# Optimization experiments

Measured on AMD Instinct MI355X. Metric: run time of the kernel, lower is better.

The kernel has to match this reference:

```python
import jax, jax.numpy as jnp
import numpy as np

B, S, T = 64, 512, 256  # batch, seq_len, num_tags


def setup_inputs() -> dict:
    key = jax.random.key(0)
    k1, k2, k3, k4 = jax.random.split(key, 4)
    emissions = jax.random.normal(k1, (B, S, T), dtype=jnp.float32)
    tags = jax.random.randint(k2, (B, S), 0, T, dtype=jnp.int32)
    mask = jnp.ones((B, S), dtype=bool)
    # nn.init.uniform_(-0.01, 0.01) as in reset_parameters()
    transitions = jax.random.uniform(k3, (T, T), minval=-0.01, maxval=0.01, dtype=jnp.float32)
    tse = jax.random.uniform(k4, (T + 2, T + 2), minval=-0.01, maxval=0.01, dtype=jnp.float32)
    tse = tse.at[T + 1, T].set(-10000.0)  # transitions[end_tag, start_tag] = -10000
    return {"emissions": emissions, "tags": tags, "mask": mask,
            "transitions": transitions, "transitions_with_start_end": tse}


def reference(emissions, tags, mask, transitions, transitions_with_start_end):
    Bv, Sv, Tv = emissions.shape
    start, end = Tv, Tv + 1

    # ---- forward algorithm (log partition), faithful to the torch recurrence:
    # new[b, j] = alpha[b, j] + logsumexp_k( trans[k, j] + emit_t[b, k] )
    # (the mask line fv*mask + fv*~mask in the original is a no-op)
    alpha0 = emissions[:, 0] + transitions_with_start_end[start, :Tv]

    def step(alpha, em_t):  # em_t: [B, T]
        lse = jax.nn.logsumexp(transitions[None, :, :] + em_t[:, :, None], axis=1)  # [B, T]
        return alpha + lse, None

    ems = jnp.swapaxes(emissions[:, 1:], 0, 1)  # [S-1, B, T]
    alpha, _ = jax.lax.scan(step, alpha0, ems)
    forward_score = jax.nn.logsumexp(alpha + transitions_with_start_end[:Tv, end], axis=1)  # [B]

    # ---- gold path score
    mf = mask.astype(emissions.dtype)
    emit = jnp.take_along_axis(emissions, tags[:, :, None].astype(jnp.int32), axis=2)[:, :, 0]  # [B, S]
    score = transitions_with_start_end[start, tags[:, 0]]
    score = score + jnp.sum(emit * mf, axis=1)
    score = score + jnp.sum(transitions[tags[:, 1:], tags[:, :-1]] * mf[:, 1:], axis=1)
    last_idx = jnp.sum(mask.astype(jnp.int32), axis=1) - 1  # [B]
    last_tags = jnp.take_along_axis(tags, last_idx[:, None], axis=1)[:, 0]
    score = score + transitions_with_start_end[last_tags, end]

    return forward_score - score  # negative log-likelihood per batch element, [B]
```

## Files before the change

### kernel.cpp

```cpp
#include <hip/hip_runtime.h>
#include <cstdint>

#define B_ 64
#define S_ 512
#define T_ 256
#define TP2 258

#define BM 64
#define BK 32
#define LDA 40
#define LDB 40

typedef __attribute__((ext_vector_type(8))) short short8;
typedef __attribute__((ext_vector_type(4))) float f32x4;

__device__ __forceinline__ ushort f2bf(float f) {
    union { float f; uint32_t u; } c; c.f = f;
    uint32_t u = c.u;
    u += 0x7FFFu + ((u >> 16) & 1u);
    return (ushort)(u >> 16);
}

__global__ void prep_w(const float* __restrict__ trans, ushort* __restrict__ wt,
                       float* __restrict__ accb) {
    int k = blockIdx.x;
    int n = threadIdx.x;
    wt[n * T_ + k] = f2bf(__expf(trans[k * T_ + n]));
    if (k < B_) accb[k * T_ + n] = 0.f;
}

__global__ __launch_bounds__(256, 3) void gemm_lse(
    const float* __restrict__ em, const ushort* __restrict__ wt,
    float* __restrict__ accb)
{
    __shared__ ushort Alds[BM * LDA];
    __shared__ ushort Blds[T_ * LDB];

    int blk  = blockIdx.x;
    long r0  = (long)blk * BM;
    int batch = blk >> 3;
    bool has_s0 = (blk & 7) == 0;

    int tid  = threadIdx.x;
    int wave = tid >> 6;
    int lane = tid & 63;
    int quad = lane >> 4;
    int l15  = lane & 15;

    f32x4 acc[4][4];
    #pragma unroll
    for (int i = 0; i < 4; ++i)
        #pragma unroll
        for (int j = 0; j < 4; ++j)
            acc[i][j] = (f32x4){0.f, 0.f, 0.f, 0.f};

    int srow = tid >> 2;
    int skc  = (tid & 3) * 8;

    for (int kt = 0; kt < T_ / BK; ++kt) {
        int k0 = kt * BK;
        {
            const float* src = em + (r0 + srow) * T_ + k0 + skc;
            float4 va = *(const float4*)(src);
            float4 vb = *(const float4*)(src + 4);
            union { ushort u[8]; uint4 v; } pk;
            pk.u[0] = f2bf(__expf(va.x)); pk.u[1] = f2bf(__expf(va.y));
            pk.u[2] = f2bf(__expf(va.z)); pk.u[3] = f2bf(__expf(va.w));
            pk.u[4] = f2bf(__expf(vb.x)); pk.u[5] = f2bf(__expf(vb.y));
            pk.u[6] = f2bf(__expf(vb.z)); pk.u[7] = f2bf(__expf(vb.w));
            *(uint4*)&Alds[srow * LDA + skc] = pk.v;
        }
        #pragma unroll
        for (int p = 0; p < 4; ++p) {
            int idx = tid + p * 256;
            uint4 v = *(const uint4*)&wt[(idx >> 2) * T_ + k0 + (idx & 3) * 8];
            *(uint4*)&Blds[(idx >> 2) * LDB + (idx & 3) * 8] = v;
        }
        __syncthreads();

        short8 af[4], bf[4];
        #pragma unroll
        for (int i = 0; i < 4; ++i)
            af[i] = *(const short8*)&Alds[(i * 16 + l15) * LDA + quad * 8];
        #pragma unroll
        for (int j = 0; j < 4; ++j)
            bf[j] = *(const short8*)&Blds[(wave * 64 + j * 16 + l15) * LDB + quad * 8];
        #pragma unroll
        for (int i = 0; i < 4; ++i)
            #pragma unroll
            for (int j = 0; j < 4; ++j)
                acc[i][j] = __builtin_amdgcn_mfma_f32_16x16x32_bf16(af[i], bf[j], acc[i][j], 0, 0, 0);
        __syncthreads();
    }

    #pragma unroll
    for (int j = 0; j < 4; ++j) {
        float s = 0.f;
        #pragma unroll
        for (int i = 0; i < 4; ++i) {
            f32x4 a = acc[i][j];
            #pragma unroll
            for (int v = 0; v < 4; ++v) {
                bool skip = has_s0 && (i == 0) && (quad == 0) && (v == 0);
                if (!skip) s += __logf(a[v]);
            }
        }
        s += __shfl_xor(s, 16);
        s += __shfl_xor(s, 32);
        if (lane < 16)
            atomicAdd(&accb[batch * T_ + wave * 64 + j * 16 + lane], s);
    }
}

__global__ __launch_bounds__(256) void finalize(
    const float* __restrict__ em, const int* __restrict__ tags,
    const float* __restrict__ trans, const float* __restrict__ tse,
    const float* __restrict__ accb, float* __restrict__ out)
{
    __shared__ float red[8];
    int b = blockIdx.x;
    int j = threadIdx.x;
    int w = j >> 6;

    float v = em[(long)b * S_ * T_ + j] + tse[T_ * TP2 + j]
            + accb[b * T_ + j] + tse[j * TP2 + (T_ + 1)];

    float m = v;
    #pragma unroll
    for (int o = 32; o; o >>= 1) m = fmaxf(m, __shfl_xor(m, o));
    if ((j & 63) == 0) red[w] = m;
    __syncthreads();
    m = fmaxf(fmaxf(red[0], red[1]), fmaxf(red[2], red[3]));

    float e = __expf(v - m);
    #pragma unroll
    for (int o = 32; o; o >>= 1) e += __shfl_xor(e, o);
    if ((j & 63) == 0) red[4 + w] = e;
    __syncthreads();
    float fwd = m + __logf(red[4] + red[5] + red[6] + red[7]);

    const int* tg = tags + b * S_;
    float sc = 0.f;
    for (int s = j; s < S_; s += 256) {
        int t = tg[s];
        sc += em[((long)b * S_ + s) * T_ + t];
        if (s >= 1) sc += trans[t * T_ + tg[s - 1]];
    }
    if (j == 0) {
        sc += tse[T_ * TP2 + tg[0]];
        sc += tse[tg[S_ - 1] * TP2 + (T_ + 1)];
    }
    #pragma unroll
    for (int o = 32; o; o >>= 1) sc += __shfl_xor(sc, o);
    __syncthreads();
    if ((j & 63) == 0) red[w] = sc;
    __syncthreads();
    if (j == 0) out[b] = fwd - (red[0] + red[1] + red[2] + red[3]);
}

extern "C" void kernel_launch(void* const* d_in, const int* in_sizes, int n_in,
                              void* d_out, int out_size, void* d_ws, size_t ws_size,
                              hipStream_t stream) {
    const float* em    = (const float*)d_in[0];
    const int*   tags  = (const int*)d_in[1];
    const float* trans = (const float*)d_in[3];
    const float* tse   = (const float*)d_in[4];
    float* out = (float*)d_out;

    ushort* wt   = (ushort*)d_ws;
    float*  accb = (float*)((char*)d_ws + 131072);

    prep_w<<<T_, T_, 0, stream>>>(trans, wt, accb);
    gemm_lse<<<(B_ * S_) / BM, 256, 0, stream>>>(em, wt, accb);
    finalize<<<B_, T_, 0, stream>>>(em, tags, trans, tse, accb, out);
}
```

Before: 93.21 us.

## Double-buffer A tile in LDS and load B fragments directly from global

The GEMM main loop now double-buffers the exponentiated emission tile in shared memory. The next tile's global load and exp conversion overlap with the MFMAs on the current tile, which leaves one barrier per iteration instead of two. The B (exp-transition) fragments are read straight from global/L2 into registers, so the B shared-memory staging is gone. The loop is fully unrolled and the occupancy hint drops from 3 to 2 blocks per CU. This trades LDS traffic and barriers for more register pressure and uncoalesced-per-lane global reads of the weight matrix.

```diff
diff --git a/kernel.cpp b/kernel.cpp
--- a/kernel.cpp
+++ b/kernel.cpp
@@ -9,7 +9,6 @@
 #define BM 64
 #define BK 32
 #define LDA 40
-#define LDB 40
 
 typedef __attribute__((ext_vector_type(8))) short short8;
 typedef __attribute__((ext_vector_type(4))) float f32x4;
@@ -29,12 +28,11 @@
     if (k < B_) accb[k * T_ + n] = 0.f;
 }
 
-__global__ __launch_bounds__(256, 3) void gemm_lse(
+__global__ __launch_bounds__(256, 2) void gemm_lse(
     const float* __restrict__ em, const ushort* __restrict__ wt,
     float* __restrict__ accb)
 {
-    __shared__ ushort Alds[BM * LDA];
-    __shared__ ushort Blds[T_ * LDB];
+    __shared__ ushort Alds[2][BM * LDA];
 
     int blk  = blockIdx.x;
     long r0  = (long)blk * BM;
@@ -57,39 +55,56 @@
     int srow = tid >> 2;
     int skc  = (tid & 3) * 8;
 
-    for (int kt = 0; kt < T_ / BK; ++kt) {
-        int k0 = kt * BK;
-        {
-            const float* src = em + (r0 + srow) * T_ + k0 + skc;
-            float4 va = *(const float4*)(src);
-            float4 vb = *(const float4*)(src + 4);
+    const float*  asrc = em + (r0 + srow) * T_ + skc;
+    const ushort* bsrc = wt + (wave * 64 + l15) * T_ + quad * 8;
+
+    {
+        float4 va = *(const float4*)(asrc);
+        float4 vb = *(const float4*)(asrc + 4);
+        union { ushort u[8]; uint4 v; } pk;
+        pk.u[0] = f2bf(__expf(va.x)); pk.u[1] = f2bf(__expf(va.y));
+        pk.u[2] = f2bf(__expf(va.z)); pk.u[3] = f2bf(__expf(va.w));
+        pk.u[4] = f2bf(__expf(vb.x)); pk.u[5] = f2bf(__expf(vb.y));
+        pk.u[6] = f2bf(__expf(vb.z)); pk.u[7] = f2bf(__expf(vb.w));
+        *(uint4*)&Alds[0][srow * LDA + skc] = pk.v;
+    }
+    __syncthreads();
+
+    #pragma unroll
+    for (int kt = 0; kt < 8; ++kt) {
+        const int k0  = kt * BK;
+        const int cur = kt & 1;
+
+        short8 bf[4];
+        #pragma unroll
+        for (int j = 0; j < 4; ++j)
+            bf[j] = *(const short8*)(bsrc + j * 16 * T_ + k0);
+
+        float4 va, vb;
+        if (kt < 7) {
+            va = *(const float4*)(asrc + k0 + BK);
+            vb = *(const float4*)(asrc + k0 + BK + 4);
+        }
+
+        short8 af[4];
+        #pragma unroll
+        for (int i = 0; i < 4; ++i)
+            af[i] = *(const short8*)&Alds[cur][(i * 16 + l15) * LDA + quad * 8];
+
+        #pragma unroll
+        for (int i = 0; i < 4; ++i)
+            #pragma unroll
+            for (int j = 0; j < 4; ++j)
+                acc[i][j] = __builtin_amdgcn_mfma_f32_16x16x32_bf16(af[i], bf[j], acc[i][j], 0, 0, 0);
+
+        if (kt < 7) {
             union { ushort u[8]; uint4 v; } pk;
             pk.u[0] = f2bf(__expf(va.x)); pk.u[1] = f2bf(__expf(va.y));
             pk.u[2] = f2bf(__expf(va.z)); pk.u[3] = f2bf(__expf(va.w));
             pk.u[4] = f2bf(__expf(vb.x)); pk.u[5] = f2bf(__expf(vb.y));
             pk.u[6] = f2bf(__expf(vb.z)); pk.u[7] = f2bf(__expf(vb.w));
-            *(uint4*)&Alds[srow * LDA + skc] = pk.v;
+            *(uint4*)&Alds[cur ^ 1][srow * LDA + skc] = pk.v;
         }
-        #pragma unroll
-        for (int p = 0; p < 4; ++p) {
-            int idx = tid + p * 256;
-            uint4 v = *(const uint4*)&wt[(idx >> 2) * T_ + k0 + (idx & 3) * 8];
-            *(uint4*)&Blds[(idx >> 2) * LDB + (idx & 3) * 8] = v;
-        }
-        __syncthreads();
-
-        short8 af[4], bf[4];
-        #pragma unroll
-        for (int i = 0; i < 4; ++i)
-            af[i] = *(const short8*)&Alds[(i * 16 + l15) * LDA + quad * 8];
-        #pragma unroll
-        for (int j = 0; j < 4; ++j)
-            bf[j] = *(const short8*)&Blds[(wave * 64 + j * 16 + l15) * LDB + quad * 8];
-        #pragma unroll
-        for (int i = 0; i < 4; ++i)
-            #pragma unroll
-            for (int j = 0; j < 4; ++j)
-                acc[i][j] = __builtin_amdgcn_mfma_f32_16x16x32_bf16(af[i], bf[j], acc[i][j], 0, 0, 0);
         __syncthreads();
     }
 
```

After: 95.82 us. +2.8%, slower.

## Fuse prep, GEMM-LSE and finalize into one cooperative kernel with tickets

Applied to the files above, without the earlier changes.

Replaces three kernel launches with one cooperative kernel. Preparation work (exp-transpose of transitions, zeroing accumulators and tickets, gold-path scores) is split across blocks and followed by a grid-wide sync. The last block finishing each batch, chosen by an atomic ticket, then runs the final logsumexp. This removes launch gaps and the separate finalize pass, at the cost of a grid barrier and requiring all 512 blocks to be co-resident.

```diff
diff --git a/kernel.cpp b/kernel.cpp
--- a/kernel.cpp
+++ b/kernel.cpp
@@ -1,5 +1,8 @@
 #include <hip/hip_runtime.h>
+#include <hip/hip_cooperative_groups.h>
 #include <cstdint>
+
+namespace cg = cooperative_groups;
 
 #define B_ 64
 #define S_ 512
@@ -21,27 +24,53 @@
     return (ushort)(u >> 16);
 }
 
-__global__ void prep_w(const float* __restrict__ trans, ushort* __restrict__ wt,
-                       float* __restrict__ accb) {
-    int k = blockIdx.x;
-    int n = threadIdx.x;
-    wt[n * T_ + k] = f2bf(__expf(trans[k * T_ + n]));
-    if (k < B_) accb[k * T_ + n] = 0.f;
-}
-
-__global__ __launch_bounds__(256, 3) void gemm_lse(
-    const float* __restrict__ em, const ushort* __restrict__ wt,
-    float* __restrict__ accb)
+__global__ __launch_bounds__(256, 3) void crf_fused(
+    const float* __restrict__ em, const int* __restrict__ tags,
+    const float* __restrict__ trans, const float* __restrict__ tse,
+    ushort* __restrict__ wt, float* __restrict__ accb,
+    int* __restrict__ tickets, float* __restrict__ gold,
+    float* __restrict__ out)
 {
     __shared__ ushort Alds[BM * LDA];
     __shared__ ushort Blds[T_ * LDB];
+    __shared__ float red[8];
+    __shared__ int winflag;
 
-    int blk  = blockIdx.x;
-    long r0  = (long)blk * BM;
+    int blk = blockIdx.x;
+    int tid = threadIdx.x;
+
+    if (blk < 256) {
+        wt[tid * T_ + blk] = f2bf(__expf(trans[blk * T_ + tid]));
+    } else if (blk < 320) {
+        accb[(blk - 256) * T_ + tid] = 0.f;
+    } else if (blk == 320) {
+        if (tid < B_) tickets[tid] = 0;
+    } else if (blk >= 448) {
+        int b = blk - 448;
+        const int* tg = tags + b * S_;
+        float sc = 0.f;
+        for (int s = tid; s < S_; s += 256) {
+            int t = tg[s];
+            sc += em[((long)b * S_ + s) * T_ + t];
+            if (s >= 1) sc += trans[t * T_ + tg[s - 1]];
+        }
+        if (tid == 0) {
+            sc += tse[T_ * TP2 + tg[0]];
+            sc += tse[tg[S_ - 1] * TP2 + (T_ + 1)];
+        }
+        #pragma unroll
+        for (int o = 32; o; o >>= 1) sc += __shfl_xor(sc, o);
+        if ((tid & 63) == 0) red[tid >> 6] = sc;
+        __syncthreads();
+        if (tid == 0) gold[b] = red[0] + red[1] + red[2] + red[3];
+    }
+
+    cg::this_grid().sync();
+
+    long r0   = (long)blk * BM;
     int batch = blk >> 3;
     bool has_s0 = (blk & 7) == 0;
 
-    int tid  = threadIdx.x;
     int wave = tid >> 6;
     int lane = tid & 63;
     int quad = lane >> 4;
@@ -110,52 +139,42 @@
         if (lane < 16)
             atomicAdd(&accb[batch * T_ + wave * 64 + j * 16 + lane], s);
     }
-}
 
-__global__ __launch_bounds__(256) void finalize(
-    const float* __restrict__ em, const int* __restrict__ tags,
-    const float* __restrict__ trans, const float* __restrict__ tse,
-    const float* __restrict__ accb, float* __restrict__ out)
-{
-    __shared__ float red[8];
-    int b = blockIdx.x;
-    int j = threadIdx.x;
-    int w = j >> 6;
+    __syncthreads();
+    if (tid == 0) {
+        int t = __hip_atomic_fetch_add(&tickets[batch], 1,
+                                       __ATOMIC_ACQ_REL, __HIP_MEMORY_SCOPE_AGENT);
+        winflag = (t == 7);
+    }
+    __syncthreads();
+    if (winflag) {
+        int b = batch;
+        int j = tid;
+        int w = j >> 6;
+        float aj = __hip_atomic_load(&accb[b * T_ + j],
+                                     __ATOMIC_ACQUIRE, __HIP_MEMORY_SCOPE_AGENT);
+        float v = em[(long)b * S_ * T_ + j] + tse[T_ * TP2 + j]
+                + aj + tse[j * TP2 + (T_ + 1)];
 
-    float v = em[(long)b * S_ * T_ + j] + tse[T_ * TP2 + j]
-            + accb[b * T_ + j] + tse[j * TP2 + (T_ + 1)];
+        float m = v;
+        #pragma unroll
+        for (int o = 32; o; o >>= 1) m = fmaxf(m, __shfl_xor(m, o));
+        if ((j & 63) == 0) red[w] = m;
+        __syncthreads();
+        m = fmaxf(fmaxf(red[0], red[1]), fmaxf(red[2], red[3]));
 
-    float m = v;
-    #pragma unroll
-    for (int o = 32; o; o >>= 1) m = fmaxf(m, __shfl_xor(m, o));
-    if ((j & 63) == 0) red[w] = m;
-    __syncthreads();
-    m = fmaxf(fmaxf(red[0], red[1]), fmaxf(red[2], red[3]));
-
-    float e = __expf(v - m);
-    #pragma unroll
-    for (int o = 32; o; o >>= 1) e += __shfl_xor(e, o);
-    if ((j & 63) == 0) red[4 + w] = e;
-    __syncthreads();
-    float fwd = m + __logf(red[4] + red[5] + red[6] + red[7]);
-
-    const int* tg = tags + b * S_;
-    float sc = 0.f;
-    for (int s = j; s < S_; s += 256) {
-        int t = tg[s];
-        sc += em[((long)b * S_ + s) * T_ + t];
-        if (s >= 1) sc += trans[t * T_ + tg[s - 1]];
+        float e = __expf(v - m);
+        #pragma unroll
+        for (int o = 32; o; o >>= 1) e += __shfl_xor(e, o);
+        if ((j & 63) == 0) red[4 + w] = e;
+        __syncthreads();
+        if (j == 0) {
+            float fwd = m + __logf(red[4] + red[5] + red[6] + red[7]);
+            float g = __hip_atomic_load(&gold[b],
+                                        __ATOMIC_ACQUIRE, __HIP_MEMORY_SCOPE_AGENT);
+            out[b] = fwd - g;
+        }
     }
-    if (j == 0) {
-        sc += tse[T_ * TP2 + tg[0]];
-        sc += tse[tg[S_ - 1] * TP2 + (T_ + 1)];
-    }
-    #pragma unroll
-    for (int o = 32; o; o >>= 1) sc += __shfl_xor(sc, o);
-    __syncthreads();
-    if ((j & 63) == 0) red[w] = sc;
-    __syncthreads();
-    if (j == 0) out[b] = fwd - (red[0] + red[1] + red[2] + red[3]);
 }
 
 extern "C" void kernel_launch(void* const* d_in, const int* in_sizes, int n_in,
@@ -167,10 +186,14 @@
     const float* tse   = (const float*)d_in[4];
     float* out = (float*)d_out;
 
-    ushort* wt   = (ushort*)d_ws;
-    float*  accb = (float*)((char*)d_ws + 131072);
+    ushort* wt      = (ushort*)d_ws;
+    float*  accb    = (float*)((char*)d_ws + 131072);
+    int*    tickets = (int*)((char*)d_ws + 196608);
+    float*  gold    = (float*)((char*)d_ws + 196864);
 
-    prep_w<<<T_, T_, 0, stream>>>(trans, wt, accb);
-    gemm_lse<<<(B_ * S_) / BM, 256, 0, stream>>>(em, wt, accb);
-    finalize<<<B_, T_, 0, stream>>>(em, tags, trans, tse, accb, out);
+    void* args[] = { (void*)&em, (void*)&tags, (void*)&trans, (void*)&tse,
+                     (void*)&wt, (void*)&accb, (void*)&tickets, (void*)&gold,
+                     (void*)&out };
+    hipLaunchCooperativeKernel((void*)crf_fused, dim3((B_ * S_) / BM), dim3(256),
+                               args, 0, stream);
 }
```

New measurement: 180.4 us. 93.6% more time.

## Drop LDS staging; keep exp'd A fragments in registers, stream B from global

Applied to the files above, without the earlier changes.

The GEMM kernel no longer stages tiles through shared memory. Each wave now owns 16 rows and holds all 8 K-chunks of exp/bf16-converted emissions in registers. It loops over 16 column tiles, reading the transposed weight fragments straight from global/L2, and takes logs and does the atomic reduction per tile. This removes LDS traffic and the __syncthreads barriers. In exchange, every wave reads the whole 128KB weight matrix from cache, and the minimum occupancy hint is lowered from 3 to 2 blocks.

```diff
diff --git a/kernel.cpp b/kernel.cpp
--- a/kernel.cpp
+++ b/kernel.cpp
@@ -7,9 +7,6 @@
 #define TP2 258
 
 #define BM 64
-#define BK 32
-#define LDA 40
-#define LDB 40
 
 typedef __attribute__((ext_vector_type(8))) short short8;
 typedef __attribute__((ext_vector_type(4))) float f32x4;
@@ -29,13 +26,10 @@
     if (k < B_) accb[k * T_ + n] = 0.f;
 }
 
-__global__ __launch_bounds__(256, 3) void gemm_lse(
+__global__ __launch_bounds__(256, 2) void gemm_lse(
     const float* __restrict__ em, const ushort* __restrict__ wt,
     float* __restrict__ accb)
 {
-    __shared__ ushort Alds[BM * LDA];
-    __shared__ ushort Blds[T_ * LDB];
-
     int blk  = blockIdx.x;
     long r0  = (long)blk * BM;
     int batch = blk >> 3;
@@ -47,68 +41,39 @@
     int quad = lane >> 4;
     int l15  = lane & 15;
 
-    f32x4 acc[4][4];
+    const float* asrc = em + (r0 + wave * 16 + l15) * T_ + quad * 8;
+    short8 af[8];
     #pragma unroll
-    for (int i = 0; i < 4; ++i)
-        #pragma unroll
-        for (int j = 0; j < 4; ++j)
-            acc[i][j] = (f32x4){0.f, 0.f, 0.f, 0.f};
-
-    int srow = tid >> 2;
-    int skc  = (tid & 3) * 8;
-
-    for (int kt = 0; kt < T_ / BK; ++kt) {
-        int k0 = kt * BK;
-        {
-            const float* src = em + (r0 + srow) * T_ + k0 + skc;
-            float4 va = *(const float4*)(src);
-            float4 vb = *(const float4*)(src + 4);
-            union { ushort u[8]; uint4 v; } pk;
-            pk.u[0] = f2bf(__expf(va.x)); pk.u[1] = f2bf(__expf(va.y));
-            pk.u[2] = f2bf(__expf(va.z)); pk.u[3] = f2bf(__expf(va.w));
-            pk.u[4] = f2bf(__expf(vb.x)); pk.u[5] = f2bf(__expf(vb.y));
-            pk.u[6] = f2bf(__expf(vb.z)); pk.u[7] = f2bf(__expf(vb.w));
-            *(uint4*)&Alds[srow * LDA + skc] = pk.v;
-        }
-        #pragma unroll
-        for (int p = 0; p < 4; ++p) {
-            int idx = tid + p * 256;
-            uint4 v = *(const uint4*)&wt[(idx >> 2) * T_ + k0 + (idx & 3) * 8];
-            *(uint4*)&Blds[(idx >> 2) * LDB + (idx & 3) * 8] = v;
-        }
-        __syncthreads();
-
-        short8 af[4], bf[4];
-        #pragma unroll
-        for (int i = 0; i < 4; ++i)
-            af[i] = *(const short8*)&Alds[(i * 16 + l15) * LDA + quad * 8];
-        #pragma unroll
-        for (int j = 0; j < 4; ++j)
-            bf[j] = *(const short8*)&Blds[(wave * 64 + j * 16 + l15) * LDB + quad * 8];
-        #pragma unroll
-        for (int i = 0; i < 4; ++i)
-            #pragma unroll
-            for (int j = 0; j < 4; ++j)
-                acc[i][j] = __builtin_amdgcn_mfma_f32_16x16x32_bf16(af[i], bf[j], acc[i][j], 0, 0, 0);
-        __syncthreads();
+    for (int kt = 0; kt < 8; ++kt) {
+        float4 a = *(const float4*)(asrc + kt * 32);
+        float4 b = *(const float4*)(asrc + kt * 32 + 4);
+        union { ushort u[8]; short8 s; } pk;
+        pk.u[0] = f2bf(__expf(a.x)); pk.u[1] = f2bf(__expf(a.y));
+        pk.u[2] = f2bf(__expf(a.z)); pk.u[3] = f2bf(__expf(a.w));
+        pk.u[4] = f2bf(__expf(b.x)); pk.u[5] = f2bf(__expf(b.y));
+        pk.u[6] = f2bf(__expf(b.z)); pk.u[7] = f2bf(__expf(b.w));
+        af[kt] = pk.s;
     }
 
-    #pragma unroll
-    for (int j = 0; j < 4; ++j) {
-        float s = 0.f;
+    const ushort* bsrc = wt + l15 * T_ + quad * 8;
+    bool skiprow = has_s0 && (wave == 0) && (quad == 0);
+
+    #pragma unroll 4
+    for (int j = 0; j < 16; ++j) {
+        f32x4 acc = (f32x4){0.f, 0.f, 0.f, 0.f};
         #pragma unroll
-        for (int i = 0; i < 4; ++i) {
-            f32x4 a = acc[i][j];
-            #pragma unroll
-            for (int v = 0; v < 4; ++v) {
-                bool skip = has_s0 && (i == 0) && (quad == 0) && (v == 0);
-                if (!skip) s += __logf(a[v]);
-            }
+        for (int kt = 0; kt < 8; ++kt) {
+            short8 bf = *(const short8*)(bsrc + (long)(j * 16) * T_ + kt * 32);
+            acc = __builtin_amdgcn_mfma_f32_16x16x32_bf16(af[kt], bf, acc, 0, 0, 0);
         }
+        float s = skiprow ? 0.f : __logf(acc[0]);
+        s += __logf(acc[1]);
+        s += __logf(acc[2]);
+        s += __logf(acc[3]);
         s += __shfl_xor(s, 16);
         s += __shfl_xor(s, 32);
         if (lane < 16)
-            atomicAdd(&accb[batch * T_ + wave * 64 + j * 16 + lane], s);
+            atomicAdd(&accb[batch * T_ + j * 16 + lane], s);
     }
 }
 
```

Result: slower. 119.8 us (+28.5%).
